# Kernel optimization log

Measured on AMD Instinct MI355X. Metric: run time of the kernel, lower is better.

## Reference

```python
import jax, jax.numpy as jnp
import numpy as np

B, DIM, L, S, E = 4096, 3, 300, 60, 128
P = L // S  # points per local region = 5


def setup_inputs() -> dict:
    key = jax.random.key(0)
    ks = jax.random.split(key, 9)
    inp = {
        "x": jax.random.normal(ks[0], (B, DIM, L), dtype=jnp.float32),
        # local_emb_nn: Conv1d(DIM, E, 1) -> weight [E, DIM], bias [E]
        "W_le": jax.random.normal(ks[1], (E, DIM), dtype=jnp.float32) * 0.1,
        "b_le": jax.random.normal(ks[2], (E,), dtype=jnp.float32) * 0.1,
        "W_lr": jax.random.normal(ks[3], (S, P), dtype=jnp.float32) * 0.1,
        "b_lr": jax.random.normal(ks[4], (S,), dtype=jnp.float32) * 0.1,
        # global_emb_nn: Conv1d(DIM, E, 1)
        "W_ge": jax.random.normal(ks[5], (E, DIM), dtype=jnp.float32) * 0.1,
        "b_ge": jax.random.normal(ks[6], (E,), dtype=jnp.float32) * 0.1,
        # global_nn: Conv1d(L, 1, 1) -> weight [L], bias scalar
        "W_gn": jax.random.normal(ks[7], (L,), dtype=jnp.float32) * 0.1,
        "b_gn": jax.random.normal(ks[8], (), dtype=jnp.float32) * 0.1,
    }
    return inp


def reference(x, W_le, b_le, W_lr, b_lr, W_ge, b_ge, W_gn, b_gn):
    # global branch: [B,DIM,L] -> [B,E,L] -> relu -> transpose [B,L,E]
    gf = jax.nn.relu(jnp.einsum('ec,bcl->ble', W_ge, x) + b_ge)
    # global_nn: 1x1 conv over L channels -> [B,E], then relu
    gf = jax.nn.relu(jnp.einsum('l,ble->be', W_gn, gf) + b_gn)
    # local branch: [B,DIM,L] -> [B,E,L] -> relu -> transpose [B,L,E]
    lf = jax.nn.relu(jnp.einsum('ec,bcl->ble', W_le, x) + b_le)
    # chunk into S regions of P points, apply per-region 1x1 conv (P->1)
    lf = lf.reshape(B, S, P, E)
    lf = jnp.einsum('sp,bspe->bse', W_lr, lf) + b_lr[None, :, None]
    # add broadcast global feature [B,1,E]
    return lf + gf[:, None, :]
```

## Files before the change

kernel.cpp:

```cpp
#include <hip/hip_runtime.h>


typedef float v2f __attribute__((ext_vector_type(2)));

#define PKFMA(a, b, c) __builtin_elementwise_fma((a), (b), (c))
#define PKRELU(a)      __builtin_elementwise_max((a), (v2f)0.0f)
#define SPLAT(s)       ((v2f)(s))

__global__ __launch_bounds__(320) void cle_kernel(
    const float* __restrict__ x,
    const float* __restrict__ W_le,
    const float* __restrict__ b_le,
    const float* __restrict__ W_lr,
    const float* __restrict__ b_lr,
    const float* __restrict__ W_ge,
    const float* __restrict__ b_ge,
    const float* __restrict__ W_gn,
    const float* __restrict__ b_gn,
    float* __restrict__ out)
{
    const int tid  = threadIdx.x;
    const int lane = tid & 63;
    const int wq   = __builtin_amdgcn_readfirstlane(tid >> 6);
    const int b    = blockIdx.x;
    const int e0   = lane << 1;

    __shared__ v2f sgp[5][64];

    const float* __restrict__ xb = x + (size_t)b * 900;

    const v2f wg0 = {W_ge[e0 * 3 + 0], W_ge[e0 * 3 + 3]};
    const v2f wg1 = {W_ge[e0 * 3 + 1], W_ge[e0 * 3 + 4]};
    const v2f wg2 = {W_ge[e0 * 3 + 2], W_ge[e0 * 3 + 5]};
    const v2f bg  = {b_ge[e0], b_ge[e0 + 1]};
    const v2f wl0 = {W_le[e0 * 3 + 0], W_le[e0 * 3 + 3]};
    const v2f wl1 = {W_le[e0 * 3 + 1], W_le[e0 * 3 + 4]};
    const v2f wl2 = {W_le[e0 * 3 + 2], W_le[e0 * 3 + 5]};
    const v2f bl  = {b_le[e0], b_le[e0 + 1]};
    const float bgn = b_gn[0];

    v2f ga0 = SPLAT(0.f), ga1 = SPLAT(0.f);
    v2f A00 = SPLAT(0.f), A01 = SPLAT(0.f), A02 = SPLAT(0.f), A03 = SPLAT(0.f);
    v2f A10 = SPLAT(0.f), A11 = SPLAT(0.f), A12 = SPLAT(0.f), A13 = SPLAT(0.f);
    v2f A20 = SPLAT(0.f), A21 = SPLAT(0.f), A22 = SPLAT(0.f), A23 = SPLAT(0.f);

#define GEj(j) PKRELU(PKFMA(wg2, SPLAT(c2##j), PKFMA(wg1, SPLAT(c1##j), PKFMA(wg0, SPLAT(c0##j), bg))))
#define LEj(j) PKRELU(PKFMA(wl2, SPLAT(c2##j), PKFMA(wl1, SPLAT(c1##j), PKFMA(wl0, SPLAT(c0##j), bl))))

#define DOQ(qi, A0, A1, A2, A3)                                                \
    {                                                                          \
        const int lq = lbase + (qi) * 4;                          \
        const float c00 = xb[lq + 0],   c01 = xb[lq + 1];                      \
        const float c02 = xb[lq + 2],   c03 = xb[lq + 3];                      \
        const float c10 = xb[300 + lq + 0], c11 = xb[300 + lq + 1];            \
        const float c12 = xb[300 + lq + 2], c13 = xb[300 + lq + 3];            \
        const float c20 = xb[600 + lq + 0], c21 = xb[600 + lq + 1];            \
        const float c22 = xb[600 + lq + 2], c23 = xb[600 + lq + 3];            \
        ga0 = PKFMA(SPLAT(W_gn[lq + 0]), GEj(0), ga0);                         \
        ga1 = PKFMA(SPLAT(W_gn[lq + 1]), GEj(1), ga1);                         \
        ga0 = PKFMA(SPLAT(W_gn[lq + 2]), GEj(2), ga0);                         \
        ga1 = PKFMA(SPLAT(W_gn[lq + 3]), GEj(3), ga1);                         \
        A0 = PKFMA(SPLAT(W_lr[lq + 0]), LEj(0), A0);                           \
        A1 = PKFMA(SPLAT(W_lr[lq + 1]), LEj(1), A1);                           \
        A2 = PKFMA(SPLAT(W_lr[lq + 2]), LEj(2), A2);                           \
        A3 = PKFMA(SPLAT(W_lr[lq + 3]), LEj(3), A3);                           \
    }

    {
        const int lbase = wq * 60;
        DOQ(0, A00, A00, A00, A00)
        DOQ(1, A00, A01, A01, A01)
        DOQ(2, A01, A01, A02, A02)
        DOQ(3, A02, A02, A02, A03)
        DOQ(4, A03, A03, A03, A03)
    }
    {
        const int lbase = wq * 60 + 20;
        DOQ(0, A10, A10, A10, A10)
        DOQ(1, A10, A11, A11, A11)
        DOQ(2, A11, A11, A12, A12)
        DOQ(3, A12, A12, A12, A13)
        DOQ(4, A13, A13, A13, A13)
    }
    {
        const int lbase = wq * 60 + 40;
        DOQ(0, A20, A20, A20, A20)
        DOQ(1, A20, A21, A21, A21)
        DOQ(2, A21, A21, A22, A22)
        DOQ(3, A22, A22, A22, A23)
        DOQ(4, A23, A23, A23, A23)
    }

    sgp[wq][lane] = ga0 + ga1;
    __syncthreads();

    v2f gf;
    {
        const v2f p0 = sgp[0][lane], p1 = sgp[1][lane], p2 = sgp[2][lane];
        const v2f p3 = sgp[3][lane], p4 = sgp[4][lane];
        gf = PKRELU((((p0 + p1) + (p2 + p3)) + p4) + SPLAT(bgn));
    }

    v2f* ob2 = (v2f*)(out + (size_t)b * (60 * 128)) + lane;
    const int s0 = wq * 12;
    ob2[(s0 +  0) * 64] = A00 + gf + SPLAT(b_lr[s0 +  0]);
    ob2[(s0 +  1) * 64] = A01 + gf + SPLAT(b_lr[s0 +  1]);
    ob2[(s0 +  2) * 64] = A02 + gf + SPLAT(b_lr[s0 +  2]);
    ob2[(s0 +  3) * 64] = A03 + gf + SPLAT(b_lr[s0 +  3]);
    ob2[(s0 +  4) * 64] = A10 + gf + SPLAT(b_lr[s0 +  4]);
    ob2[(s0 +  5) * 64] = A11 + gf + SPLAT(b_lr[s0 +  5]);
    ob2[(s0 +  6) * 64] = A12 + gf + SPLAT(b_lr[s0 +  6]);
    ob2[(s0 +  7) * 64] = A13 + gf + SPLAT(b_lr[s0 +  7]);
    ob2[(s0 +  8) * 64] = A20 + gf + SPLAT(b_lr[s0 +  8]);
    ob2[(s0 +  9) * 64] = A21 + gf + SPLAT(b_lr[s0 +  9]);
    ob2[(s0 + 10) * 64] = A22 + gf + SPLAT(b_lr[s0 + 10]);
    ob2[(s0 + 11) * 64] = A23 + gf + SPLAT(b_lr[s0 + 11]);
}

extern "C" void kernel_launch(void* const* d_in, const int* in_sizes, int n_in,
                              void* d_out, int out_size, void* d_ws, size_t ws_size,
                              hipStream_t stream) {
    const float* x    = (const float*)d_in[0];
    const float* W_le = (const float*)d_in[1];
    const float* b_le = (const float*)d_in[2];
    const float* W_lr = (const float*)d_in[3];
    const float* b_lr = (const float*)d_in[4];
    const float* W_ge = (const float*)d_in[5];
    const float* b_ge = (const float*)d_in[6];
    const float* W_gn = (const float*)d_in[7];
    const float* b_gn = (const float*)d_in[8];
    float* out = (float*)d_out;

    cle_kernel<<<4096, 320, 0, stream>>>(x, W_le, b_le, W_lr, b_lr,
                                         W_ge, b_ge, W_gn, b_gn, out);
}
```

Measured before the change: 46.35 us.

## Split global and local branches into two kernels via workspace buffer

Splits the fused kernel in two. The first kernel computes the global feature per batch, staging x in shared memory with float4 loads across 4 waves, and writes it to workspace. The second kernel runs one 64-thread block per (region group, batch) for the local branch and adds the stored global feature. This removes the in-block barrier that forced all five waves to wait before writing. In exchange it reads x twice, adds a workspace round-trip and a second launch, and creates many tiny blocks.

```diff
diff --git a/kernel.cpp b/kernel.cpp
--- a/kernel.cpp
+++ b/kernel.cpp
@@ -7,17 +7,13 @@
 #define PKRELU(a)      __builtin_elementwise_max((a), (v2f)0.0f)
 #define SPLAT(s)       ((v2f)(s))
 
-__global__ __launch_bounds__(320) void cle_kernel(
+__global__ __launch_bounds__(256) void cle_global(
     const float* __restrict__ x,
-    const float* __restrict__ W_le,
-    const float* __restrict__ b_le,
-    const float* __restrict__ W_lr,
-    const float* __restrict__ b_lr,
     const float* __restrict__ W_ge,
     const float* __restrict__ b_ge,
     const float* __restrict__ W_gn,
     const float* __restrict__ b_gn,
-    float* __restrict__ out)
+    float* __restrict__ gf_out)
 {
     const int tid  = threadIdx.x;
     const int lane = tid & 63;
@@ -25,26 +21,77 @@
     const int b    = blockIdx.x;
     const int e0   = lane << 1;
 
-    __shared__ v2f sgp[5][64];
+    __shared__ __align__(16) float4 sx4[225];
+    __shared__ v2f sgp[4][64];
 
-    const float* __restrict__ xb = x + (size_t)b * 900;
+    if (tid < 225) sx4[tid] = ((const float4*)(x + (size_t)b * 900))[tid];
 
     const v2f wg0 = {W_ge[e0 * 3 + 0], W_ge[e0 * 3 + 3]};
     const v2f wg1 = {W_ge[e0 * 3 + 1], W_ge[e0 * 3 + 4]};
     const v2f wg2 = {W_ge[e0 * 3 + 2], W_ge[e0 * 3 + 5]};
     const v2f bg  = {b_ge[e0], b_ge[e0 + 1]};
+    const float bgn = b_gn[0];
+
+    __syncthreads();
+
+#define GE(cmp) PKRELU(PKFMA(wg2, SPLAT(c2.cmp), PKFMA(wg1, SPLAT(c1.cmp), PKFMA(wg0, SPLAT(c0.cmp), bg))))
+
+    v2f ga0 = SPLAT(0.f), ga1 = SPLAT(0.f), ga2 = SPLAT(0.f), ga3 = SPLAT(0.f);
+    {
+        const int qb = wq * 20;
+        const int nq = (wq < 3) ? 20 : 15;
+        for (int g = 0; g < 4; ++g) {
+            if (g * 5 < nq) {
+#pragma unroll
+                for (int qi = 0; qi < 5; ++qi) {
+                    const int qq = qb + g * 5 + qi;
+                    const int l4 = qq * 4;
+                    const float4 c0 = sx4[qq], c1 = sx4[75 + qq], c2 = sx4[150 + qq];
+                    ga0 = PKFMA(SPLAT(W_gn[l4 + 0]), GE(x), ga0);
+                    ga1 = PKFMA(SPLAT(W_gn[l4 + 1]), GE(y), ga1);
+                    ga2 = PKFMA(SPLAT(W_gn[l4 + 2]), GE(z), ga2);
+                    ga3 = PKFMA(SPLAT(W_gn[l4 + 3]), GE(w), ga3);
+                }
+            }
+        }
+    }
+    sgp[wq][lane] = (ga0 + ga1) + (ga2 + ga3);
+    __syncthreads();
+
+    if (wq == 0) {
+        const v2f p0 = sgp[0][lane], p1 = sgp[1][lane];
+        const v2f p2 = sgp[2][lane], p3 = sgp[3][lane];
+        const v2f gf = PKRELU(((p0 + p1) + (p2 + p3)) + SPLAT(bgn));
+        ((v2f*)gf_out)[(size_t)b * 64 + lane] = gf;
+    }
+}
+
+__global__ __launch_bounds__(64) void cle_local(
+    const float* __restrict__ x,
+    const float* __restrict__ W_le,
+    const float* __restrict__ b_le,
+    const float* __restrict__ W_lr,
+    const float* __restrict__ b_lr,
+    const float* __restrict__ gf_in,
+    float* __restrict__ out)
+{
+    const int lane = threadIdx.x;
+    const int t    = blockIdx.x;
+    const int b    = blockIdx.y;
+    const int e0   = lane << 1;
+
+    const float* __restrict__ xb = x + (size_t)b * 900;
+
     const v2f wl0 = {W_le[e0 * 3 + 0], W_le[e0 * 3 + 3]};
     const v2f wl1 = {W_le[e0 * 3 + 1], W_le[e0 * 3 + 4]};
     const v2f wl2 = {W_le[e0 * 3 + 2], W_le[e0 * 3 + 5]};
     const v2f bl  = {b_le[e0], b_le[e0 + 1]};
-    const float bgn = b_gn[0];
+    const v2f gf  = ((const v2f*)gf_in)[(size_t)b * 64 + lane];
 
-    v2f ga0 = SPLAT(0.f), ga1 = SPLAT(0.f);
     v2f A00 = SPLAT(0.f), A01 = SPLAT(0.f), A02 = SPLAT(0.f), A03 = SPLAT(0.f);
     v2f A10 = SPLAT(0.f), A11 = SPLAT(0.f), A12 = SPLAT(0.f), A13 = SPLAT(0.f);
     v2f A20 = SPLAT(0.f), A21 = SPLAT(0.f), A22 = SPLAT(0.f), A23 = SPLAT(0.f);
 
-#define GEj(j) PKRELU(PKFMA(wg2, SPLAT(c2##j), PKFMA(wg1, SPLAT(c1##j), PKFMA(wg0, SPLAT(c0##j), bg))))
 #define LEj(j) PKRELU(PKFMA(wl2, SPLAT(c2##j), PKFMA(wl1, SPLAT(c1##j), PKFMA(wl0, SPLAT(c0##j), bl))))
 
 #define DOQ(qi, A0, A1, A2, A3)                                                \
@@ -56,10 +103,6 @@
         const float c12 = xb[300 + lq + 2], c13 = xb[300 + lq + 3];            \
         const float c20 = xb[600 + lq + 0], c21 = xb[600 + lq + 1];            \
         const float c22 = xb[600 + lq + 2], c23 = xb[600 + lq + 3];            \
-        ga0 = PKFMA(SPLAT(W_gn[lq + 0]), GEj(0), ga0);                         \
-        ga1 = PKFMA(SPLAT(W_gn[lq + 1]), GEj(1), ga1);                         \
-        ga0 = PKFMA(SPLAT(W_gn[lq + 2]), GEj(2), ga0);                         \
-        ga1 = PKFMA(SPLAT(W_gn[lq + 3]), GEj(3), ga1);                         \
         A0 = PKFMA(SPLAT(W_lr[lq + 0]), LEj(0), A0);                           \
         A1 = PKFMA(SPLAT(W_lr[lq + 1]), LEj(1), A1);                           \
         A2 = PKFMA(SPLAT(W_lr[lq + 2]), LEj(2), A2);                           \
@@ -67,7 +110,7 @@
     }
 
     {
-        const int lbase = wq * 60;
+        const int lbase = t * 60;
         DOQ(0, A00, A00, A00, A00)
         DOQ(1, A00, A01, A01, A01)
         DOQ(2, A01, A01, A02, A02)
@@ -75,7 +118,7 @@
         DOQ(4, A03, A03, A03, A03)
     }
     {
-        const int lbase = wq * 60 + 20;
+        const int lbase = t * 60 + 20;
         DOQ(0, A10, A10, A10, A10)
         DOQ(1, A10, A11, A11, A11)
         DOQ(2, A11, A11, A12, A12)
@@ -83,7 +126,7 @@
         DOQ(4, A13, A13, A13, A13)
     }
     {
-        const int lbase = wq * 60 + 40;
+        const int lbase = t * 60 + 40;
         DOQ(0, A20, A20, A20, A20)
         DOQ(1, A20, A21, A21, A21)
         DOQ(2, A21, A21, A22, A22)
@@ -91,18 +134,8 @@
         DOQ(4, A23, A23, A23, A23)
     }
 
-    sgp[wq][lane] = ga0 + ga1;
-    __syncthreads();
-
-    v2f gf;
-    {
-        const v2f p0 = sgp[0][lane], p1 = sgp[1][lane], p2 = sgp[2][lane];
-        const v2f p3 = sgp[3][lane], p4 = sgp[4][lane];
-        gf = PKRELU((((p0 + p1) + (p2 + p3)) + p4) + SPLAT(bgn));
-    }
-
     v2f* ob2 = (v2f*)(out + (size_t)b * (60 * 128)) + lane;
-    const int s0 = wq * 12;
+    const int s0 = t * 12;
     ob2[(s0 +  0) * 64] = A00 + gf + SPLAT(b_lr[s0 +  0]);
     ob2[(s0 +  1) * 64] = A01 + gf + SPLAT(b_lr[s0 +  1]);
     ob2[(s0 +  2) * 64] = A02 + gf + SPLAT(b_lr[s0 +  2]);
@@ -130,7 +163,8 @@
     const float* W_gn = (const float*)d_in[7];
     const float* b_gn = (const float*)d_in[8];
     float* out = (float*)d_out;
+    float* gf  = (float*)d_ws;
 
-    cle_kernel<<<4096, 320, 0, stream>>>(x, W_le, b_le, W_lr, b_lr,
-                                         W_ge, b_ge, W_gn, b_gn, out);
+    cle_global<<<4096, 256, 0, stream>>>(x, W_ge, b_ge, W_gn, b_gn, gf);
+    cle_local <<<dim3(5, 4096), 64, 0, stream>>>(x, W_le, b_le, W_lr, b_lr, gf, out);
 }
```

Result: slower. 50.90 us (+9.8%).
